# Performance work log

Hardware: AMD Instinct MI355X
Metric: run time of the kernel (lower is better)

The kernel has to match this reference:

```python
import jax, jax.numpy as jnp
import numpy as np


def setup_inputs() -> dict:
    key = jax.random.key(0)
    ks = jax.random.split(key, 12)
    B, H, C, D, G, F = 2, 32, 256, 128, 2048, 128
    inp = {
        'k_c': jax.random.normal(ks[0], (B, H, C, D), jnp.float32),
        'v_c': jax.random.normal(ks[1], (B, H, C, D), jnp.float32),
        'fk_c': jax.random.uniform(ks[2], (B, H, C, F), jnp.float32),
        'score_c': jax.random.uniform(ks[3], (B, H, C), jnp.float32),
        'K_win': jax.random.normal(ks[4], (B, H, C, D), jnp.float32),
        'V_win': jax.random.normal(ks[5], (B, H, C, D), jnp.float32),
        'K_top': jax.random.normal(ks[6], (B, H, G, D), jnp.float32),
        'V_top': jax.random.normal(ks[7], (B, H, G, D), jnp.float32),
        'FK_top': jax.random.uniform(ks[8], (B, H, G, F), jnp.float32),
        'heap_val': jax.random.uniform(ks[9], (B, H, G), jnp.float32),
        'heap_idx': jax.random.randint(ks[10], (B, H, G), 0, 2048, jnp.int32),
        'tokens_seen': 4096,
    }
    return inp


def reference(k_c, v_c, fk_c, score_c, K_win, V_win, K_top, V_top, FK_top,
              heap_val, heap_idx, tokens_seen):
    # Steady-state LoLAState.train_chunk (heap and window already populated).
    B, H, C, D = k_c.shape
    G = heap_val.shape[-1]

    # Sliding window: drop oldest slot, append last token of chunk.
    K_win_new = jnp.concatenate([K_win[:, :, 1:], k_c[:, :, -1:]], axis=2)
    V_win_new = jnp.concatenate([V_win[:, :, 1:], v_c[:, :, -1:]], axis=2)

    # Global token indices for this chunk.
    chunk_idx = jnp.broadcast_to(
        (tokens_seen + jnp.arange(C, dtype=heap_idx.dtype))[None, None, :], (B, H, C))

    # Top-G eviction over [old heap | new chunk scores].
    cat_val = jnp.concatenate([heap_val, score_c], axis=-1)   # [B,H,G+C]
    cat_idx = jnp.concatenate([heap_idx, chunk_idx], axis=-1)  # [B,H,G+C]
    new_val, sel = jax.lax.top_k(cat_val, G)                   # sel in [0, G+C)
    new_idx = jnp.take_along_axis(cat_idx, sel, axis=-1)

    # Gather survivors from [old top | new chunk].
    prefix_K = jnp.concatenate([K_top, k_c], axis=2)    # [B,H,G+C,D]
    prefix_V = jnp.concatenate([V_top, v_c], axis=2)
    prefix_FK = jnp.concatenate([FK_top, fk_c], axis=2)
    sel4 = sel[..., None]
    K_top_new = jnp.take_along_axis(prefix_K, sel4, axis=2)
    V_top_new = jnp.take_along_axis(prefix_V, sel4, axis=2)
    FK_top_new = jnp.take_along_axis(prefix_FK, sel4, axis=2)

    # Low-rank sums (fp32, matching _recompute_sums).
    H_sum = jnp.einsum('bhgf,bhgd->bhfd', FK_top_new.astype(jnp.float32),
                       V_top_new.astype(jnp.float32))
    S_sum = FK_top_new.astype(jnp.float32).sum(axis=2)

    return (K_win_new, V_win_new, K_top_new, V_top_new, FK_top_new,
            new_val, new_idx, H_sum, S_sum)
```

## Files before the change

kernel.cpp:

```cpp
#include <hip/hip_runtime.h>
#include <stdint.h>

#define BB 2
#define HH 32
#define CC 256
#define DD 128
#define GG 2048
#define FF 128
#define NCAT (GG + CC)

__global__ __launch_bounds__(256) void rank_topk_kernel(
    const float* __restrict__ heap_val, const int* __restrict__ heap_idx,
    const float* __restrict__ score_c, const int* __restrict__ tokens_seen,
    float* __restrict__ out_val, float* __restrict__ out_idx,
    int* __restrict__ selws)
{
    __shared__ uint64_t keys[NCAT];

    const int blk = blockIdx.x;
    const int bh  = blk / 9;
    const int seg = blk - bh * 9;
    const int tid = threadIdx.x;

    const float* hv = heap_val + (size_t)bh * GG;
    const float* sc = score_c  + (size_t)bh * CC;

    for (int i = tid; i < NCAT; i += 256) {
        uint32_t fb = (i < GG) ? __float_as_uint(hv[i])
                               : __float_as_uint(sc[i - GG]);
        keys[i] = ((uint64_t)fb << 12) | (uint64_t)(4095 - i);
    }
    __syncthreads();

    const int cand = seg * 256 + tid;
    const uint64_t my = keys[cand];

    int rank = 0;
    const ulonglong2* k2 = (const ulonglong2*)keys;
#pragma unroll 4
    for (int j = 0; j < NCAT / 2; ++j) {
        ulonglong2 p = k2[j];
        rank += (p.x > my) + (p.y > my);
    }

    if (rank < GG) {
        const size_t o = (size_t)bh * GG + rank;
        out_val[o] = __uint_as_float((uint32_t)(my >> 12));
        int j = 4095 - (int)(my & 0xFFFull);
        int gidx = (j < GG) ? heap_idx[(size_t)bh * GG + j]
                            : (tokens_seen[0] + (j - GG));
        out_idx[o] = (float)gidx;
        selws[o] = j;
    }
}

__global__ __launch_bounds__(512) void fused_gather_hsum_kernel(
    const float4* __restrict__ K_top, const float4* __restrict__ V_top,
    const float4* __restrict__ FK_top,
    const float4* __restrict__ k_c, const float4* __restrict__ v_c,
    const float4* __restrict__ fk_c,
    const int* __restrict__ selws,
    float4* __restrict__ oK, float4* __restrict__ oV, float4* __restrict__ oFK,
    float* __restrict__ Hpart, float* __restrict__ Spart, int nseg)
{
    __shared__ float fk_t[32][128];
    __shared__ float v_t[32][128];
    __shared__ float4 sredA[512];
    __shared__ float4 sredB[512];

    const int rows_pb = GG / nseg;
    const int ntiles  = rows_pb / 32;
    const int bh  = blockIdx.x / nseg;
    const int seg = blockIdx.x - bh * nseg;
    const int tid = threadIdx.x;
    const int r   = tid >> 4;
    const int q   = tid & 15;
    const int tf  = tid >> 5;
    const int td  = tid & 31;

    const long long topQ = (long long)bh * GG * 32;
    const long long chkQ = (long long)bh * CC * 32;
    const int row0 = seg * rows_pb;
    const int selbase = bh * GG + row0;

    float acc[8][4];
#pragma unroll
    for (int a = 0; a < 8; ++a)
#pragma unroll
        for (int b2 = 0; b2 < 4; ++b2) acc[a][b2] = 0.f;
    float4 sA = make_float4(0.f, 0.f, 0.f, 0.f);
    float4 sB = make_float4(0.f, 0.f, 0.f, 0.f);

    int j = selws[selbase + r];
    const float4* bK = (j < GG) ? K_top  + topQ + (long long)j * 32
                                : k_c    + chkQ + (long long)(j - GG) * 32;
    const float4* bV = (j < GG) ? V_top  + topQ + (long long)j * 32
                                : v_c    + chkQ + (long long)(j - GG) * 32;
    const float4* bF = (j < GG) ? FK_top + topQ + (long long)j * 32
                                : fk_c   + chkQ + (long long)(j - GG) * 32;
    float4 pk0 = bK[q], pk1 = bK[q + 16];
    float4 pv0 = bV[q], pv1 = bV[q + 16];
    float4 pf0 = bF[q], pf1 = bF[q + 16];

    for (int tile = 0; tile < ntiles; ++tile) {
        const int gr = row0 + tile * 32;
        int jn = 0;
        if (tile < ntiles - 1) jn = selws[selbase + (tile + 1) * 32 + r];

        __syncthreads();
        *(float4*)&fk_t[r][q * 4]        = pf0;
        *(float4*)&fk_t[r][(q + 16) * 4] = pf1;
        *(float4*)&v_t[r][q * 4]         = pv0;
        *(float4*)&v_t[r][(q + 16) * 4]  = pv1;
        const long long ob = ((long long)bh * GG + gr + r) * 32;
        oFK[ob + q] = pf0;  oFK[ob + q + 16] = pf1;
        oV[ob + q]  = pv0;  oV[ob + q + 16]  = pv1;
        oK[ob + q]  = pk0;  oK[ob + q + 16]  = pk1;
        sA.x += pf0.x; sA.y += pf0.y; sA.z += pf0.z; sA.w += pf0.w;
        sB.x += pf1.x; sB.y += pf1.y; sB.z += pf1.z; sB.w += pf1.w;
        __syncthreads();

        if (tile < ntiles - 1) {
            const float4* nK = (jn < GG) ? K_top  + topQ + (long long)jn * 32
                                         : k_c    + chkQ + (long long)(jn - GG) * 32;
            const float4* nV = (jn < GG) ? V_top  + topQ + (long long)jn * 32
                                         : v_c    + chkQ + (long long)(jn - GG) * 32;
            const float4* nF = (jn < GG) ? FK_top + topQ + (long long)jn * 32
                                         : fk_c   + chkQ + (long long)(jn - GG) * 32;
            pk0 = nK[q]; pk1 = nK[q + 16];
            pv0 = nV[q]; pv1 = nV[q + 16];
            pf0 = nF[q]; pf1 = nF[q + 16];
        }

#pragma unroll 4
        for (int g = 0; g < 32; ++g) {
            float4 fa0 = *(const float4*)&fk_t[g][tf * 8];
            float4 fa1 = *(const float4*)&fk_t[g][tf * 8 + 4];
            float4 vvq = *(const float4*)&v_t[g][td * 4];
            float fa[8] = {fa0.x, fa0.y, fa0.z, fa0.w, fa1.x, fa1.y, fa1.z, fa1.w};
            float vv[4] = {vvq.x, vvq.y, vvq.z, vvq.w};
#pragma unroll
            for (int a = 0; a < 8; ++a)
#pragma unroll
                for (int b2 = 0; b2 < 4; ++b2)
                    acc[a][b2] += fa[a] * vv[b2];
        }
    }

    float* Hb = Hpart + (long long)blockIdx.x * (FF * DD);
#pragma unroll
    for (int a = 0; a < 8; ++a)
        *(float4*)&Hb[(long long)(tf * 8 + a) * DD + td * 4] =
            make_float4(acc[a][0], acc[a][1], acc[a][2], acc[a][3]);

    __syncthreads();
    sredA[tid] = sA; sredB[tid] = sB;
    __syncthreads();
    if (tid < 16) {
        float4 a = make_float4(0.f, 0.f, 0.f, 0.f);
        float4 b = make_float4(0.f, 0.f, 0.f, 0.f);
#pragma unroll
        for (int k = 0; k < 32; ++k) {
            float4 pa = sredA[k * 16 + tid];
            float4 pb = sredB[k * 16 + tid];
            a.x += pa.x; a.y += pa.y; a.z += pa.z; a.w += pa.w;
            b.x += pb.x; b.y += pb.y; b.z += pb.z; b.w += pb.w;
        }
        float* Sb = Spart + (long long)blockIdx.x * FF;
        *(float4*)&Sb[tid * 4]        = a;
        *(float4*)&Sb[(tid + 16) * 4] = b;
    }
}

__global__ __launch_bounds__(256) void finish_kernel(
    const float4* __restrict__ Hpart4, const float4* __restrict__ Spart4,
    const float4* __restrict__ K_win, const float4* __restrict__ V_win,
    const float4* __restrict__ k_c, const float4* __restrict__ v_c,
    float4* __restrict__ oKw, float4* __restrict__ oVw,
    float4* __restrict__ oH, float4* __restrict__ oS, int nseg)
{
    const int b = blockIdx.x;
    const int tid = threadIdx.x;

    if (b < 4096) {
        const int QPA = BB * HH * CC * 32;
        int t = b * 256 + tid;
        int arr = t / QPA;
        int rem = t - arr * QPA;
        int row = rem >> 5;
        int q   = rem & 31;
        int bh  = row >> 8;
        int c   = row & 255;
        const float4* win = arr ? V_win : K_win;
        const float4* chk = arr ? v_c : k_c;
        float4 val = (c < CC - 1)
            ? win[((long long)bh * CC + c + 1) * 32 + q]
            : chk[((long long)bh * CC + (CC - 1)) * 32 + q];
        (arr ? oVw : oKw)[(long long)row * 32 + q] = val;
    } else if (b < 4096 + 1024) {
        int p  = (b - 4096) * 256 + tid;
        int bh = p >> 12;
        int off = p & 4095;
        float4 s = make_float4(0.f, 0.f, 0.f, 0.f);
        for (int s4 = 0; s4 < nseg; ++s4) {
            float4 v = Hpart4[(((long long)bh * nseg + s4) << 12) + off];
            s.x += v.x; s.y += v.y; s.z += v.z; s.w += v.w;
        }
        oH[p] = s;
    } else {
        int p = (b - 5120) * 256 + tid;
        int bh = p >> 5;
        int off = p & 31;
        float4 s = make_float4(0.f, 0.f, 0.f, 0.f);
        for (int s4 = 0; s4 < nseg; ++s4) {
            float4 v = Spart4[((long long)bh * nseg + s4) * 32 + off];
            s.x += v.x; s.y += v.y; s.z += v.z; s.w += v.w;
        }
        oS[p] = s;
    }
}

__global__ __launch_bounds__(256) void gather_topk_kernel(
    const float4* __restrict__ K_top, const float4* __restrict__ V_top,
    const float4* __restrict__ FK_top,
    const float4* __restrict__ k_c, const float4* __restrict__ v_c,
    const float4* __restrict__ fk_c,
    const int* __restrict__ selws,
    float4* __restrict__ oK, float4* __restrict__ oV, float4* __restrict__ oFK)
{
    const long long ROWQ = (long long)BB * HH * GG * 32;
    long long t = (long long)blockIdx.x * 256 + threadIdx.x;
    int arr = (int)(t / ROWQ);
    long long rem = t - (long long)arr * ROWQ;
    int row = (int)(rem >> 5);
    int q   = (int)(rem & 31);
    int bh  = row >> 11;
    int j   = selws[row];

    const float4* topsrc = (arr == 0) ? K_top : ((arr == 1) ? V_top : FK_top);
    const float4* chksrc = (arr == 0) ? k_c   : ((arr == 1) ? v_c   : fk_c);
    float4*       dst    = (arr == 0) ? oK    : ((arr == 1) ? oV    : oFK);

    float4 val;
    if (j < GG) val = topsrc[((long long)bh * GG + j) * 32 + q];
    else        val = chksrc[((long long)bh * CC + (j - GG)) * 32 + q];
    dst[(long long)row * 32 + q] = val;
}

__global__ __launch_bounds__(256) void window_kernel(
    const float4* __restrict__ K_win, const float4* __restrict__ V_win,
    const float4* __restrict__ k_c, const float4* __restrict__ v_c,
    float4* __restrict__ oKw, float4* __restrict__ oVw)
{
    const int QPA = BB * HH * CC * 32;
    int t = blockIdx.x * 256 + threadIdx.x;
    int arr = t / QPA;
    int rem = t - arr * QPA;
    int row = rem >> 5;
    int q   = rem & 31;
    int bh  = row >> 8;
    int c   = row & 255;

    const float4* win = arr ? V_win : K_win;
    const float4* chk = arr ? v_c : k_c;
    float4 val = (c < CC - 1)
        ? win[((long long)bh * CC + c + 1) * 32 + q]
        : chk[((long long)bh * CC + (CC - 1)) * 32 + q];
    (arr ? oVw : oKw)[(long long)row * 32 + q] = val;
}

__global__ __launch_bounds__(256) void hsum_kernel(
    const float4* __restrict__ FKq, const float4* __restrict__ Vq,
    float* __restrict__ H_out, float* __restrict__ S_out)
{
    __shared__ float fk_t[32][68];
    __shared__ float v_t[32][68];
    __shared__ float4 s4[256];

    const int bx  = blockIdx.x;
    const int bh  = bx >> 2;
    const int fq  = (bx >> 1) & 1;
    const int dq  = bx & 1;
    const int tid = threadIdx.x;
    const int g0 = tid >> 4;
    const int f4 = tid & 15;

    const float4* fkb = FKq + (long long)bh * GG * 32 + fq * 16 + f4;
    const float4* vb  = Vq  + (long long)bh * GG * 32 + dq * 16 + f4;

    float acc[4][4];
#pragma unroll
    for (int a = 0; a < 4; ++a)
#pragma unroll
        for (int b2 = 0; b2 < 4; ++b2) acc[a][b2] = 0.f;
    float4 s_acc = make_float4(0.f, 0.f, 0.f, 0.f);
    const int tf = tid >> 4, td = tid & 15;

    float4 pf_fk0 = fkb[(long long)(g0)      * 32];
    float4 pf_fk1 = fkb[(long long)(g0 + 16) * 32];
    float4 pf_v0  = vb [(long long)(g0)      * 32];
    float4 pf_v1  = vb [(long long)(g0 + 16) * 32];

    for (int c0 = 0; c0 < GG; c0 += 32) {
        __syncthreads();
        *(float4*)&fk_t[g0][f4 * 4]      = pf_fk0;
        *(float4*)&fk_t[g0 + 16][f4 * 4] = pf_fk1;
        *(float4*)&v_t[g0][f4 * 4]       = pf_v0;
        *(float4*)&v_t[g0 + 16][f4 * 4]  = pf_v1;
        s_acc.x += pf_fk0.x + pf_fk1.x;
        s_acc.y += pf_fk0.y + pf_fk1.y;
        s_acc.z += pf_fk0.z + pf_fk1.z;
        s_acc.w += pf_fk0.w + pf_fk1.w;
        __syncthreads();

        if (c0 + 32 < GG) {
            pf_fk0 = fkb[(long long)(c0 + 32 + g0)      * 32];
            pf_fk1 = fkb[(long long)(c0 + 32 + g0 + 16) * 32];
            pf_v0  = vb [(long long)(c0 + 32 + g0)      * 32];
            pf_v1  = vb [(long long)(c0 + 32 + g0 + 16) * 32];
        }

#pragma unroll 4
        for (int g = 0; g < 32; ++g) {
            float fa[4], vv[4];
#pragma unroll
            for (int a = 0; a < 4; ++a) fa[a] = fk_t[g][tf * 4 + a];
#pragma unroll
            for (int b2 = 0; b2 < 4; ++b2) vv[b2] = v_t[g][td * 4 + b2];
#pragma unroll
            for (int a = 0; a < 4; ++a)
#pragma unroll
                for (int b2 = 0; b2 < 4; ++b2)
                    acc[a][b2] += fa[a] * vv[b2];
        }
    }

    float* Hb = H_out + (long long)bh * FF * DD
              + (long long)(fq * 64 + tf * 4) * DD + dq * 64 + td * 4;
#pragma unroll
    for (int a = 0; a < 4; ++a)
        *(float4*)&Hb[(long long)a * DD] =
            make_float4(acc[a][0], acc[a][1], acc[a][2], acc[a][3]);

    s4[tid] = s_acc;
    __syncthreads();
    if (dq == 0 && tid < 16) {
        float4 s = make_float4(0.f, 0.f, 0.f, 0.f);
#pragma unroll
        for (int r = 0; r < 16; ++r) {
            float4 p = s4[r * 16 + tid];
            s.x += p.x; s.y += p.y; s.z += p.z; s.w += p.w;
        }
        *(float4*)&S_out[(long long)bh * FF + fq * 64 + tid * 4] = s;
    }
}

extern "C" void kernel_launch(void* const* d_in, const int* in_sizes, int n_in,
                              void* d_out, int out_size, void* d_ws, size_t ws_size,
                              hipStream_t stream) {
    const float* k_c      = (const float*)d_in[0];
    const float* v_c      = (const float*)d_in[1];
    const float* fk_c     = (const float*)d_in[2];
    const float* score_c  = (const float*)d_in[3];
    const float* K_win    = (const float*)d_in[4];
    const float* V_win    = (const float*)d_in[5];
    const float* K_top    = (const float*)d_in[6];
    const float* V_top    = (const float*)d_in[7];
    const float* FK_top   = (const float*)d_in[8];
    const float* heap_val = (const float*)d_in[9];
    const int*   heap_idx = (const int*)d_in[10];
    const int*   tokens   = (const int*)d_in[11];

    float* out = (float*)d_out;

    const size_t SZ_WIN = (size_t)BB * HH * CC * DD;
    const size_t SZ_TOP = (size_t)BB * HH * GG * DD;
    const size_t SZ_VAL = (size_t)BB * HH * GG;
    const size_t SZ_H   = (size_t)BB * HH * FF * DD;

    float* o_Kwin  = out;
    float* o_Vwin  = o_Kwin  + SZ_WIN;
    float* o_Ktop  = o_Vwin  + SZ_WIN;
    float* o_Vtop  = o_Ktop  + SZ_TOP;
    float* o_FKtop = o_Vtop  + SZ_TOP;
    float* o_val   = o_FKtop + SZ_TOP;
    float* o_idx   = o_val   + SZ_VAL;
    float* o_H     = o_idx   + SZ_VAL;
    float* o_S     = o_H     + SZ_H;

    const size_t selN = (size_t)BB * HH * GG;

    int nseg = 8;
    size_t need8 = selN * sizeof(int)
                 + (size_t)(BB * HH * 8) * (FF * DD + FF) * sizeof(float);
    size_t need4 = selN * sizeof(int)
                 + (size_t)(BB * HH * 4) * (FF * DD + FF) * sizeof(float);
    if (ws_size < need8) nseg = 4;

    int*   selws = (int*)d_ws;
    float* Hpart = (float*)(selws + selN);
    float* Spart = Hpart + (size_t)(BB * HH * nseg) * FF * DD;

    rank_topk_kernel<<<BB * HH * 9, 256, 0, stream>>>(
        heap_val, heap_idx, score_c, tokens, o_val, o_idx, selws);

    if (ws_size >= need4) {
        fused_gather_hsum_kernel<<<BB * HH * nseg, 512, 0, stream>>>(
            (const float4*)K_top, (const float4*)V_top, (const float4*)FK_top,
            (const float4*)k_c, (const float4*)v_c, (const float4*)fk_c,
            selws, (float4*)o_Ktop, (float4*)o_Vtop, (float4*)o_FKtop,
            Hpart, Spart, nseg);

        finish_kernel<<<4096 + 1024 + 8, 256, 0, stream>>>(
            (const float4*)Hpart, (const float4*)Spart,
            (const float4*)K_win, (const float4*)V_win,
            (const float4*)k_c, (const float4*)v_c,
            (float4*)o_Kwin, (float4*)o_Vwin, (float4*)o_H, (float4*)o_S, nseg);
    } else {
        long long nthreads = 3LL * BB * HH * GG * 32;
        gather_topk_kernel<<<(int)(nthreads / 256), 256, 0, stream>>>(
            (const float4*)K_top, (const float4*)V_top, (const float4*)FK_top,
            (const float4*)k_c, (const float4*)v_c, (const float4*)fk_c,
            selws, (float4*)o_Ktop, (float4*)o_Vtop, (float4*)o_FKtop);
        int nthreads2 = 2 * BB * HH * CC * 32;
        window_kernel<<<nthreads2 / 256, 256, 0, stream>>>(
            (const float4*)K_win, (const float4*)V_win,
            (const float4*)k_c, (const float4*)v_c,
            (float4*)o_Kwin, (float4*)o_Vwin);
        hsum_kernel<<<4 * BB * HH, 256, 0, stream>>>(
            (const float4*)o_FKtop, (const float4*)o_Vtop, o_H, o_S);
    }
}
```

Before: 158.8 us.

## Replace selection gather with rank-indexed scatter over concatenated candidates

The rank kernel now stores each candidate's rank, and the fused kernel walks the G+C candidates in source order instead of gathering by selected index. Selected rows are read contiguously and scattered to their rank position, while evicted rows load as zeros so they contribute nothing to the H and S sums. This makes reads coalesced and in order and drops the dependent index load before each gather. The cost is about 12% more rows per block (2304 vs 2048) and scattered, data-dependent writes.

```diff
diff --git a/kernel.cpp b/kernel.cpp
--- a/kernel.cpp
+++ b/kernel.cpp
@@ -13,7 +13,7 @@
     const float* __restrict__ heap_val, const int* __restrict__ heap_idx,
     const float* __restrict__ score_c, const int* __restrict__ tokens_seen,
     float* __restrict__ out_val, float* __restrict__ out_idx,
-    int* __restrict__ selws)
+    int* __restrict__ rankws, int* __restrict__ selws)
 {
     __shared__ uint64_t keys[NCAT];
 
@@ -43,23 +43,24 @@
         rank += (p.x > my) + (p.y > my);
     }
 
+    rankws[(size_t)bh * NCAT + cand] = rank;
+
     if (rank < GG) {
         const size_t o = (size_t)bh * GG + rank;
         out_val[o] = __uint_as_float((uint32_t)(my >> 12));
-        int j = 4095 - (int)(my & 0xFFFull);
-        int gidx = (j < GG) ? heap_idx[(size_t)bh * GG + j]
-                            : (tokens_seen[0] + (j - GG));
+        int gidx = (cand < GG) ? heap_idx[(size_t)bh * GG + cand]
+                               : (tokens_seen[0] + (cand - GG));
         out_idx[o] = (float)gidx;
-        selws[o] = j;
-    }
-}
-
-__global__ __launch_bounds__(512) void fused_gather_hsum_kernel(
+        if (selws) selws[o] = cand;
+    }
+}
+
+__global__ __launch_bounds__(512) void fused_scatter_hsum_kernel(
     const float4* __restrict__ K_top, const float4* __restrict__ V_top,
     const float4* __restrict__ FK_top,
     const float4* __restrict__ k_c, const float4* __restrict__ v_c,
     const float4* __restrict__ fk_c,
-    const int* __restrict__ selws,
+    const int* __restrict__ rankws,
     float4* __restrict__ oK, float4* __restrict__ oV, float4* __restrict__ oFK,
     float* __restrict__ Hpart, float* __restrict__ Spart, int nseg)
 {
@@ -68,7 +69,7 @@
     __shared__ float4 sredA[512];
     __shared__ float4 sredB[512];
 
-    const int rows_pb = GG / nseg;
+    const int rows_pb = NCAT / nseg;
     const int ntiles  = rows_pb / 32;
     const int bh  = blockIdx.x / nseg;
     const int seg = blockIdx.x - bh * nseg;
@@ -81,7 +82,7 @@
     const long long topQ = (long long)bh * GG * 32;
     const long long chkQ = (long long)bh * CC * 32;
     const int row0 = seg * rows_pb;
-    const int selbase = bh * GG + row0;
+    const int rbase = bh * NCAT + row0;
 
     float acc[8][4];
 #pragma unroll
@@ -90,46 +91,61 @@
         for (int b2 = 0; b2 < 4; ++b2) acc[a][b2] = 0.f;
     float4 sA = make_float4(0.f, 0.f, 0.f, 0.f);
     float4 sB = make_float4(0.f, 0.f, 0.f, 0.f);
-
-    int j = selws[selbase + r];
-    const float4* bK = (j < GG) ? K_top  + topQ + (long long)j * 32
-                                : k_c    + chkQ + (long long)(j - GG) * 32;
-    const float4* bV = (j < GG) ? V_top  + topQ + (long long)j * 32
-                                : v_c    + chkQ + (long long)(j - GG) * 32;
-    const float4* bF = (j < GG) ? FK_top + topQ + (long long)j * 32
-                                : fk_c   + chkQ + (long long)(j - GG) * 32;
-    float4 pk0 = bK[q], pk1 = bK[q + 16];
-    float4 pv0 = bV[q], pv1 = bV[q + 16];
-    float4 pf0 = bF[q], pf1 = bF[q + 16];
+    const float4 z = make_float4(0.f, 0.f, 0.f, 0.f);
+
+    int curRk = rankws[rbase + r];
+    bool curSel = (curRk < GG);
+    float4 pk0 = z, pk1 = z, pv0 = z, pv1 = z, pf0 = z, pf1 = z;
+    {
+        int j = row0 + r;
+        if (curSel) {
+            const float4* bK = (j < GG) ? K_top  + topQ + (long long)j * 32
+                                        : k_c    + chkQ + (long long)(j - GG) * 32;
+            const float4* bV = (j < GG) ? V_top  + topQ + (long long)j * 32
+                                        : v_c    + chkQ + (long long)(j - GG) * 32;
+            const float4* bF = (j < GG) ? FK_top + topQ + (long long)j * 32
+                                        : fk_c   + chkQ + (long long)(j - GG) * 32;
+            pk0 = bK[q]; pk1 = bK[q + 16];
+            pv0 = bV[q]; pv1 = bV[q + 16];
+            pf0 = bF[q]; pf1 = bF[q + 16];
+        }
+    }
 
     for (int tile = 0; tile < ntiles; ++tile) {
-        const int gr = row0 + tile * 32;
-        int jn = 0;
-        if (tile < ntiles - 1) jn = selws[selbase + (tile + 1) * 32 + r];
-
         __syncthreads();
         *(float4*)&fk_t[r][q * 4]        = pf0;
         *(float4*)&fk_t[r][(q + 16) * 4] = pf1;
         *(float4*)&v_t[r][q * 4]         = pv0;
         *(float4*)&v_t[r][(q + 16) * 4]  = pv1;
-        const long long ob = ((long long)bh * GG + gr + r) * 32;
-        oFK[ob + q] = pf0;  oFK[ob + q + 16] = pf1;
-        oV[ob + q]  = pv0;  oV[ob + q + 16]  = pv1;
-        oK[ob + q]  = pk0;  oK[ob + q + 16]  = pk1;
         sA.x += pf0.x; sA.y += pf0.y; sA.z += pf0.z; sA.w += pf0.w;
         sB.x += pf1.x; sB.y += pf1.y; sB.z += pf1.z; sB.w += pf1.w;
         __syncthreads();
 
+        if (curSel) {
+            const long long ob = ((long long)bh * GG + curRk) * 32;
+            oFK[ob + q] = pf0;  oFK[ob + q + 16] = pf1;
+            oV[ob + q]  = pv0;  oV[ob + q + 16]  = pv1;
+            oK[ob + q]  = pk0;  oK[ob + q + 16]  = pk1;
+        }
+
         if (tile < ntiles - 1) {
-            const float4* nK = (jn < GG) ? K_top  + topQ + (long long)jn * 32
-                                         : k_c    + chkQ + (long long)(jn - GG) * 32;
-            const float4* nV = (jn < GG) ? V_top  + topQ + (long long)jn * 32
-                                         : v_c    + chkQ + (long long)(jn - GG) * 32;
-            const float4* nF = (jn < GG) ? FK_top + topQ + (long long)jn * 32
-                                         : fk_c   + chkQ + (long long)(jn - GG) * 32;
-            pk0 = nK[q]; pk1 = nK[q + 16];
-            pv0 = nV[q]; pv1 = nV[q + 16];
-            pf0 = nF[q]; pf1 = nF[q + 16];
+            int rk2 = rankws[rbase + (tile + 1) * 32 + r];
+            bool sel2 = (rk2 < GG);
+            float4 nk0 = z, nk1 = z, nv0 = z, nv1 = z, nf0 = z, nf1 = z;
+            if (sel2) {
+                int j2 = row0 + (tile + 1) * 32 + r;
+                const float4* bK = (j2 < GG) ? K_top  + topQ + (long long)j2 * 32
+                                             : k_c    + chkQ + (long long)(j2 - GG) * 32;
+                const float4* bV = (j2 < GG) ? V_top  + topQ + (long long)j2 * 32
+                                             : v_c    + chkQ + (long long)(j2 - GG) * 32;
+                const float4* bF = (j2 < GG) ? FK_top + topQ + (long long)j2 * 32
+                                             : fk_c   + chkQ + (long long)(j2 - GG) * 32;
+                nk0 = bK[q]; nk1 = bK[q + 16];
+                nv0 = bV[q]; nv1 = bV[q + 16];
+                nf0 = bF[q]; nf1 = bF[q + 16];
+            }
+            pk0 = nk0; pk1 = nk1; pv0 = nv0; pv1 = nv1; pf0 = nf0; pf1 = nf1;
+            curRk = rk2; curSel = sel2;
         }
 
 #pragma unroll 4
@@ -388,27 +404,30 @@
     float* o_H     = o_idx   + SZ_VAL;
     float* o_S     = o_H     + SZ_H;
 
-    const size_t selN = (size_t)BB * HH * GG;
-
-    int nseg = 8;
-    size_t need8 = selN * sizeof(int)
-                 + (size_t)(BB * HH * 8) * (FF * DD + FF) * sizeof(float);
-    size_t need4 = selN * sizeof(int)
-                 + (size_t)(BB * HH * 4) * (FF * DD + FF) * sizeof(float);
-    if (ws_size < need8) nseg = 4;
-
-    int*   selws = (int*)d_ws;
-    float* Hpart = (float*)(selws + selN);
-    float* Spart = Hpart + (size_t)(BB * HH * nseg) * FF * DD;
+    const size_t rankN = (size_t)BB * HH * NCAT;
+
+    auto need = [&](int ns) {
+        return rankN * sizeof(int)
+             + (size_t)(BB * HH * ns) * (FF * DD + FF) * sizeof(float);
+    };
+    int nseg = 0;
+    if (ws_size >= need(8)) nseg = 8;
+    else if (ws_size >= need(4)) nseg = 4;
+
+    int*   rankws = (int*)d_ws;
+    int*   selws  = rankws + rankN;
+    float* Hpart  = (float*)(rankws + rankN);
+    float* Spart  = Hpart + (size_t)(BB * HH * (nseg ? nseg : 1)) * FF * DD;
 
     rank_topk_kernel<<<BB * HH * 9, 256, 0, stream>>>(
-        heap_val, heap_idx, score_c, tokens, o_val, o_idx, selws);
-
-    if (ws_size >= need4) {
-        fused_gather_hsum_kernel<<<BB * HH * nseg, 512, 0, stream>>>(
+        heap_val, heap_idx, score_c, tokens, o_val, o_idx,
+        rankws, nseg ? nullptr : selws);
+
+    if (nseg) {
+        fused_scatter_hsum_kernel<<<BB * HH * nseg, 512, 0, stream>>>(
             (const float4*)K_top, (const float4*)V_top, (const float4*)FK_top,
             (const float4*)k_c, (const float4*)v_c, (const float4*)fk_c,
-            selws, (float4*)o_Ktop, (float4*)o_Vtop, (float4*)o_FKtop,
+            rankws, (float4*)o_Ktop, (float4*)o_Vtop, (float4*)o_FKtop,
             Hpart, Spart, nseg);
 
         finish_kernel<<<4096 + 1024 + 8, 256, 0, stream>>>(
```

New measurement: 160.2 us. Within noise of the previous version (+0.9%).
